# Optimization experiments

Hardware: AMD Instinct MI355X
Metric: run time of the kernel (lower is better)

## Reference

```python
import jax, jax.numpy as jnp
import numpy as np

NUM_HEADS = 16
HEAD_DIM = 64  # hidden_size 1024 / 16 heads


def setup_inputs() -> dict:
    key = jax.random.key(0)
    ks = jax.random.split(key, 4)
    B, S, H = 2, 2048, 1024
    scale = 1.0 / np.sqrt(H)
    return {
        "hidden_states": jax.random.normal(ks[0], (B, S, H), dtype=jnp.float32),
        "attention_mask": jnp.zeros((B, 1, 1, S), dtype=jnp.float32),
        "Wq": jax.random.normal(ks[1], (H, H), dtype=jnp.float32) * scale,
        "bq": jnp.zeros((H,), dtype=jnp.float32),
        "Wk": jax.random.normal(ks[2], (H, H), dtype=jnp.float32) * scale,
        "bk": jnp.zeros((H,), dtype=jnp.float32),
        "Wv": jax.random.normal(ks[3], (H, H), dtype=jnp.float32) * scale,
        "bv": jnp.zeros((H,), dtype=jnp.float32),
    }


def reference(hidden_states, attention_mask, Wq, bq, Wk, bk, Wv, bv):
    B, S, H = hidden_states.shape
    h, d = NUM_HEADS, HEAD_DIM

    def heads(x):  # [B,S,H] -> [B,h,S,d]
        return x.reshape(B, S, h, d).transpose(0, 2, 1, 3)

    q = heads(hidden_states @ Wq + bq)
    k = heads(hidden_states @ Wk + bk)
    v = heads(hidden_states @ Wv + bv)

    # [B,h,S,S] scores, scaled then additive-masked (HF BERT semantics)
    scores = jnp.einsum("bhqd,bhkd->bhqk", q, k) / jnp.sqrt(jnp.float32(d))
    scores = scores + attention_mask
    probs = jax.nn.softmax(scores, axis=-1)  # dropout p=0 -> identity

    ctx = jnp.einsum("bhqk,bhkd->bhqd", probs, v)
    ctx = ctx.transpose(0, 2, 1, 3).reshape(B, S, H)
    return ctx
```

## Files before the change

kernel.cpp:

```cpp
#include <hip/hip_runtime.h>
#include <hip/hip_bf16.h>


#define SEQ   2048
#define HID   1024
#define NHEAD 16
#define HD    64
#define SD    ((size_t)SEQ * HD)

typedef __bf16 bf16x8 __attribute__((ext_vector_type(8)));
typedef float  f32x4  __attribute__((ext_vector_type(4)));

#define L2E 1.4426950408889634f
#define SOFT_OFF 16.0f

__device__ __forceinline__ unsigned short f2b(float f) {
    unsigned int x = __float_as_uint(f);
    x += 0x7FFFu + ((x >> 16) & 1u);
    return (unsigned short)(x >> 16);
}

__device__ __forceinline__ void gload16(const unsigned short* g,
                                        unsigned short* l) {
    __builtin_amdgcn_global_load_lds(
        (const __attribute__((address_space(1))) unsigned int*)g,
        (__attribute__((address_space(3))) unsigned int*)l, 16, 0, 0);
}

__global__ __launch_bounds__(256) void cvt_x_k(const float* __restrict__ X,
                                               unsigned short* __restrict__ Xb)
{
    const size_t i = ((size_t)blockIdx.x * 256 + threadIdx.x) * 4;
    const float4 v = *(const float4*)(X + i);
    ushort4 o;
    o.x = f2b(v.x); o.y = f2b(v.y); o.z = f2b(v.z); o.w = f2b(v.w);
    *(ushort4*)(Xb + i) = o;
}

__global__ __launch_bounds__(256) void cvt_w_k(
    const float* __restrict__ Wq, const float* __restrict__ Wk,
    const float* __restrict__ Wv, unsigned short* __restrict__ Wtb)
{
    __shared__ __align__(16) unsigned short T[64][68];
    const int z = blockIdx.z;
    const float* __restrict__ W = (z == 0) ? Wq : (z == 1) ? Wk : Wv;
    const int k0 = blockIdx.x * 64, n0 = blockIdx.y * 64;
    const int tid = threadIdx.x;
    #pragma unroll
    for (int it = 0; it < 16; ++it) {
        const int idx = 256 * it + tid;
        const int r = idx >> 6, c = idx & 63;
        T[c][r] = f2b(W[(size_t)(k0 + r) * HID + n0 + c]);
    }
    __syncthreads();
    unsigned short* dst = Wtb + (size_t)z * HID * HID;
    #pragma unroll
    for (int it = 0; it < 4; ++it) {
        const int idx = 256 * it + tid;
        const int n = idx >> 4, c4 = (idx & 15) * 4;
        *(ushort4*)(dst + (size_t)(n0 + n) * HID + k0 + c4) = *(ushort4*)&T[n][c4];
    }
}

__global__ __launch_bounds__(256) void qkv_gemm_fused(
    const unsigned short* __restrict__ Xb, const unsigned short* __restrict__ Wtb,
    const float* __restrict__ bq, const float* __restrict__ bk,
    const float* __restrict__ bv, unsigned short* __restrict__ scratch)
{
    __shared__ __align__(16) unsigned char pool[40960];
    unsigned short (*Xs)[128][32] = (unsigned short (*)[128][32])pool;
    unsigned short (*Ws)[3][64][32] = (unsigned short (*)[3][64][32])(pool + 16384);

    const int orig = blockIdx.x;
    const int wg = ((orig & 7) << 6) + (orig >> 3);
    const int m0 = (wg & 31) * 128, n0 = (wg >> 5) * 64;

    const int tid = threadIdx.x, w = tid >> 6, lane = tid & 63;
    const int ln = lane & 15, quad = lane >> 4;
    const int wr = (w >> 1) * 64;
    const int wc = (w & 1) * 32;

    f32x4 acc[3][4][2];
    #pragma unroll
    for (int z = 0; z < 3; ++z)
        #pragma unroll
        for (int i = 0; i < 4; ++i)
            #pragma unroll
            for (int j = 0; j < 2; ++j) acc[z][i][j] = (f32x4){0.f, 0.f, 0.f, 0.f};

    #define STAGE(BUF, K0) { \
        _Pragma("unroll") for (int j = 0; j < 2; ++j) { \
            const int L = w * 128 + j * 64 + lane; \
            unsigned short* l = &Xs[BUF][0][0] + (size_t)(w * 128 + j * 64) * 8; \
            gload16(Xb + (size_t)(m0 + (L >> 2)) * HID + (K0) + (L & 3) * 8, l); \
        } \
        _Pragma("unroll") for (int j = 0; j < 3; ++j) { \
            const int L = w * 192 + j * 64 + lane; \
            const int z_ = L >> 8, r_ = (L & 255) >> 2, c_ = (L & 3) * 8; \
            unsigned short* l = &Ws[BUF][0][0][0] + (size_t)(w * 192 + j * 64) * 8; \
            gload16(Wtb + (size_t)z_ * HID * HID + (size_t)(n0 + r_) * HID + (K0) + c_, l); \
        } }

    STAGE(0, 0);

    int cur = 0;
    for (int k0 = 0; k0 < HID; k0 += 32) {
        __syncthreads();
        if (k0 + 32 < HID) {
            const int nxt = cur ^ 1;
            STAGE(nxt, k0 + 32);
        }

        bf16x8 am[4];
        #pragma unroll
        for (int t = 0; t < 4; ++t)
            am[t] = *(const bf16x8*)&Xs[cur][wr + t * 16 + ln][quad * 8];
        #pragma unroll
        for (int z = 0; z < 3; ++z) {
            bf16x8 bn[2];
            #pragma unroll
            for (int n = 0; n < 2; ++n)
                bn[n] = *(const bf16x8*)&Ws[cur][z][wc + n * 16 + ln][quad * 8];
            #pragma unroll
            for (int mt = 0; mt < 4; ++mt)
                #pragma unroll
                for (int nt = 0; nt < 2; ++nt)
                    acc[z][mt][nt] = __builtin_amdgcn_mfma_f32_16x16x32_bf16(
                        am[mt], bn[nt], acc[z][mt][nt], 0, 0, 0);
        }
        cur ^= 1;
    }
    #undef STAGE

    __syncthreads();
    const int b = m0 >> 11;
    const int srow0 = (m0 + wr) & (SEQ - 1);
    const int head = (n0 + wc) >> 6;
    const int dimb = (n0 + wc) & 63;

    unsigned short (*EtQ)[36] = (unsigned short (*)[36])(pool + (size_t)w * 4352);
    #pragma unroll
    for (int z = 0; z < 2; ++z) {
        const float* __restrict__ Bp = (z == 0) ? bq : bk;
        float bias[2];
        #pragma unroll
        for (int nt = 0; nt < 2; ++nt) bias[nt] = Bp[n0 + wc + nt * 16 + ln];
        #pragma unroll
        for (int half = 0; half < 2; ++half) {
            #pragma unroll
            for (int mt2 = 0; mt2 < 2; ++mt2) {
                const int mt = half * 2 + mt2;
                #pragma unroll
                for (int nt = 0; nt < 2; ++nt)
                    #pragma unroll
                    for (int r = 0; r < 4; ++r)
                        EtQ[mt2 * 16 + quad * 4 + r][nt * 16 + ln] =
                            f2b(acc[z][mt][nt][r] + bias[nt]);
            }
            #pragma unroll
            for (int it = 0; it < 4; ++it) {
                const int row = it * 8 + (lane >> 3), c4 = (lane & 7) * 4;
                *(ushort4*)(scratch +
                    ((size_t)(z * 32 + b * NHEAD + head) * SEQ + srow0
                     + half * 32 + row) * HD + dimb + c4) =
                    *(const ushort4*)&EtQ[row][c4];
            }
        }
    }
    {
        unsigned short (*EtV)[68] = (unsigned short (*)[68])(pool + (size_t)w * 4352);
        float bias[2];
        #pragma unroll
        for (int nt = 0; nt < 2; ++nt) bias[nt] = bv[n0 + wc + nt * 16 + ln];
        #pragma unroll
        for (int nt = 0; nt < 2; ++nt)
            #pragma unroll
            for (int mt = 0; mt < 4; ++mt) {
                ushort4 o;
                o.x = f2b(acc[2][mt][nt][0] + bias[nt]);
                o.y = f2b(acc[2][mt][nt][1] + bias[nt]);
                o.z = f2b(acc[2][mt][nt][2] + bias[nt]);
                o.w = f2b(acc[2][mt][nt][3] + bias[nt]);
                *(ushort4*)&EtV[nt * 16 + ln][mt * 16 + quad * 4] = o;
            }
        #pragma unroll
        for (int it = 0; it < 8; ++it) {
            const int d = it * 4 + quad, s4 = ln * 4;
            *(ushort4*)(scratch +
                ((size_t)(64 + b * NHEAD + head) * HD + dimb + d) * SEQ
                + srow0 + s4) = *(const ushort4*)&EtV[d][s4];
        }
    }
}

__device__ __forceinline__ void gemm_epilogue(
    f32x4 acc[4][4], const float* __restrict__ Bp,
    unsigned short* __restrict__ scratch, unsigned short (*Et)[68],
    int z, int m0, int n0, int wr, int wc, int ln, int quad)
{
    const int b = m0 >> 11;
    const int srow0 = (m0 + wr) & (SEQ - 1);
    const int head = (n0 + wc) >> 6;
    __syncthreads();

    if (z == 2) {
        #pragma unroll
        for (int half = 0; half < 2; ++half) {
            #pragma unroll
            for (int nt2 = 0; nt2 < 2; ++nt2) {
                const int nt = half * 2 + nt2;
                const float bias = Bp[n0 + wc + nt * 16 + ln];
                #pragma unroll
                for (int mt = 0; mt < 4; ++mt) {
                    ushort4 o;
                    o.x = f2b(acc[mt][nt][0] + bias);
                    o.y = f2b(acc[mt][nt][1] + bias);
                    o.z = f2b(acc[mt][nt][2] + bias);
                    o.w = f2b(acc[mt][nt][3] + bias);
                    *(ushort4*)&Et[nt2 * 16 + ln][mt * 16 + quad * 4] = o;
                }
            }
            __syncthreads();
            #pragma unroll
            for (int it = 0; it < 8; ++it) {
                const int d = it * 4 + quad, s4 = ln * 4;
                *(ushort4*)(scratch +
                    ((size_t)(64 + b * NHEAD + head) * HD + half * 32 + d) * SEQ
                    + srow0 + s4) = *(const ushort4*)&Et[d][s4];
            }
            __syncthreads();
        }
    } else {
        #pragma unroll
        for (int half = 0; half < 2; ++half) {
            #pragma unroll
            for (int mt2 = 0; mt2 < 2; ++mt2) {
                const int mt = half * 2 + mt2;
                #pragma unroll
                for (int nt = 0; nt < 4; ++nt) {
                    const float bias = Bp[n0 + wc + nt * 16 + ln];
                    #pragma unroll
                    for (int r = 0; r < 4; ++r)
                        Et[mt2 * 16 + quad * 4 + r][nt * 16 + ln] =
                            f2b(acc[mt][nt][r] + bias);
                }
            }
            __syncthreads();
            #pragma unroll
            for (int it = 0; it < 8; ++it) {
                const int r = it * 4 + quad, c4 = ln * 4;
                *(ushort4*)(scratch +
                    ((size_t)(z * 32 + b * NHEAD + head) * SEQ + srow0
                     + half * 32 + r) * HD + c4) = *(const ushort4*)&Et[r][c4];
            }
            __syncthreads();
        }
    }
}

__global__ __launch_bounds__(256) void qkv_gemm_fp32(
    const float* __restrict__ X,
    const float* __restrict__ Wq, const float* __restrict__ bq,
    const float* __restrict__ Wk, const float* __restrict__ bk,
    const float* __restrict__ Wv, const float* __restrict__ bv,
    unsigned short* __restrict__ scratch)
{
    __shared__ __align__(16) unsigned char pool[20480];
    unsigned short (*Xs)[40] = (unsigned short (*)[40])pool;
    unsigned short (*Wt)[40] = (unsigned short (*)[40])(pool + 10240);

    const int z = blockIdx.z;
    const float* __restrict__ W  = (z == 0) ? Wq : (z == 1) ? Wk : Wv;
    const float* __restrict__ Bp = (z == 0) ? bq : (z == 1) ? bk : bv;

    const int tid = threadIdx.x, w = tid >> 6, lane = tid & 63;
    const int ln = lane & 15, quad = lane >> 4;
    const int wr = (w >> 1) * 64, wc = (w & 1) * 64;
    const int m0 = blockIdx.x * 128, n0 = blockIdx.y * 128;

    const int xr = tid >> 3, xc = (tid & 7) * 4;
    const int wkr = tid >> 5, wnc = (tid & 31) * 4;

    f32x4 acc[4][4];
    #pragma unroll
    for (int i = 0; i < 4; ++i)
        #pragma unroll
        for (int j = 0; j < 4; ++j) acc[i][j] = (f32x4){0.f, 0.f, 0.f, 0.f};

    for (int k0 = 0; k0 < HID; k0 += 32) {
        __syncthreads();
        #pragma unroll
        for (int it = 0; it < 4; ++it) {
            const int r = xr + 32 * it;
            const float4 xv = *(const float4*)(X + (size_t)(m0 + r) * HID + k0 + xc);
            ushort4 xb;
            xb.x = f2b(xv.x); xb.y = f2b(xv.y); xb.z = f2b(xv.z); xb.w = f2b(xv.w);
            *(ushort4*)&Xs[r][xc] = xb;
            const int kr = wkr + 8 * it;
            const float4 wv = *(const float4*)(W + (size_t)(k0 + kr) * HID + n0 + wnc);
            Wt[wnc + 0][kr] = f2b(wv.x);
            Wt[wnc + 1][kr] = f2b(wv.y);
            Wt[wnc + 2][kr] = f2b(wv.z);
            Wt[wnc + 3][kr] = f2b(wv.w);
        }
        __syncthreads();
        bf16x8 am[4], bn[4];
        #pragma unroll
        for (int t = 0; t < 4; ++t) {
            am[t] = *(const bf16x8*)&Xs[wr + t * 16 + ln][quad * 8];
            bn[t] = *(const bf16x8*)&Wt[wc + t * 16 + ln][quad * 8];
        }
        #pragma unroll
        for (int mt = 0; mt < 4; ++mt)
            #pragma unroll
            for (int nt = 0; nt < 4; ++nt)
                acc[mt][nt] = __builtin_amdgcn_mfma_f32_16x16x32_bf16(
                    am[mt], bn[nt], acc[mt][nt], 0, 0, 0);
    }
    unsigned short (*Et)[68] = (unsigned short (*)[68])(pool + (size_t)w * 4352);
    gemm_epilogue(acc, Bp, scratch, Et, z, m0, n0, wr, wc, ln, quad);
}

__global__ __launch_bounds__(256) void attn_mfma(
    const unsigned short* __restrict__ scratch,
    const float* __restrict__ mask,
    float* __restrict__ out)
{
    __shared__ __align__(16) unsigned char smem[37888];
    unsigned short (*Ks)[64][72] = (unsigned short (*)[64][72])smem;
    unsigned short (*Vt)[64][72] = (unsigned short (*)[64][72])(smem + 18432);
    float* lrbuf = (float*)(smem + 36864);
    float (*OA)[68] = (float (*)[68])smem;
    float (*OB)[68] = (float (*)[68])(smem + 18432);

    const int orig = blockIdx.x;
    const int wg = ((orig & 7) << 7) + (orig >> 3);
    const int qt = wg & 31;
    const int bh = wg >> 5;
    const int b = bh >> 4, head = bh & 15;

    const unsigned short* __restrict__ Qp  = scratch + (size_t)bh * SD;
    const unsigned short* __restrict__ Kp  = scratch + (size_t)(32 + bh) * SD;
    const unsigned short* __restrict__ Vtp = scratch + (size_t)(64 + bh) * SD;
    const float* __restrict__ maskp = mask + b * SEQ;

    const int tid = threadIdx.x, w = tid >> 6, lane = tid & 63;
    const int ln = lane & 15, quad = lane >> 4;
    const int wk0 = w * 16;

    bf16x8 qb[4][2];
    #pragma unroll
    for (int t = 0; t < 4; ++t)
        #pragma unroll
        for (int h = 0; h < 2; ++h)
            qb[t][h] = *(const bf16x8*)(Qp +
                (size_t)(qt * 64 + t * 16 + ln) * HD + h * 32 + quad * 8);

    f32x4 O[4][4];
    #pragma unroll
    for (int i = 0; i < 4; ++i)
        #pragma unroll
        for (int j = 0; j < 4; ++j) O[i][j] = (f32x4){0.f, 0.f, 0.f, 0.f};
    float lr[4] = {0.f, 0.f, 0.f, 0.f};

    const int sr8 = tid >> 3, sc8 = (tid & 7) * 8;

    {
        uint4 a = *(const uint4*)(Kp + (size_t)sr8 * HD + sc8);
        uint4 c = *(const uint4*)(Kp + (size_t)(sr8 + 32) * HD + sc8);
        uint4 d = *(const uint4*)(Vtp + (size_t)sr8 * SEQ + sc8);
        uint4 e = *(const uint4*)(Vtp + (size_t)(sr8 + 32) * SEQ + sc8);
        *(uint4*)&Ks[0][sr8][sc8]      = a;
        *(uint4*)&Ks[0][sr8 + 32][sc8] = c;
        *(uint4*)&Vt[0][sr8][sc8]      = d;
        *(uint4*)&Vt[0][sr8 + 32][sc8] = e;
    }
    uint4 kg0 = *(const uint4*)(Kp + (size_t)(64 + sr8) * HD + sc8);
    uint4 kg1 = *(const uint4*)(Kp + (size_t)(64 + sr8 + 32) * HD + sc8);
    uint4 vg0 = *(const uint4*)(Vtp + (size_t)sr8 * SEQ + 64 + sc8);
    uint4 vg1 = *(const uint4*)(Vtp + (size_t)(sr8 + 32) * SEQ + 64 + sc8);
    __syncthreads();

    const float cc = 0.125f * L2E;

    for (int kt = 0; kt < 32; ++kt) {
        const int cur = kt & 1;
        if (kt < 31) {
            *(uint4*)&Ks[cur ^ 1][sr8][sc8]      = kg0;
            *(uint4*)&Ks[cur ^ 1][sr8 + 32][sc8] = kg1;
            *(uint4*)&Vt[cur ^ 1][sr8][sc8]      = vg0;
            *(uint4*)&Vt[cur ^ 1][sr8 + 32][sc8] = vg1;
        }
        if (kt < 30) {
            const int kn = kt + 2;
            kg0 = *(const uint4*)(Kp + (size_t)(kn * 64 + sr8) * HD + sc8);
            kg1 = *(const uint4*)(Kp + (size_t)(kn * 64 + sr8 + 32) * HD + sc8);
            vg0 = *(const uint4*)(Vtp + (size_t)sr8 * SEQ + kn * 64 + sc8);
            vg1 = *(const uint4*)(Vtp + (size_t)(sr8 + 32) * SEQ + kn * 64 + sc8);
        }

        const bf16x8 ka0 = *(const bf16x8*)&Ks[cur][wk0 + ln][quad * 8];
        const bf16x8 ka1 = *(const bf16x8*)&Ks[cur][wk0 + ln][32 + quad * 8];

        uint2 vl[4];
        #pragma unroll
        for (int dg = 0; dg < 4; ++dg)
            vl[dg] = *(const uint2*)&Vt[cur][dg * 16 + ln][wk0 + quad * 4];

        f32x4 s[4];
        #pragma unroll
        for (int t = 0; t < 4; ++t) {
            f32x4 a = (f32x4){0.f, 0.f, 0.f, 0.f};
            a = __builtin_amdgcn_mfma_f32_16x16x32_bf16(ka0, qb[t][0], a, 0, 0, 0);
            a = __builtin_amdgcn_mfma_f32_16x16x32_bf16(ka1, qb[t][1], a, 0, 0, 0);
            s[t] = a;
        }

        const float4 mk4 = *(const float4*)(maskp + kt * 64 + wk0 + quad * 4);
        const float b0 = fmaf(mk4.x, L2E, -SOFT_OFF);
        const float b1 = fmaf(mk4.y, L2E, -SOFT_OFF);
        const float b2 = fmaf(mk4.z, L2E, -SOFT_OFF);
        const float b3 = fmaf(mk4.w, L2E, -SOFT_OFF);

        bf16x8 pb[4];
        #pragma unroll
        for (int t = 0; t < 4; ++t) {
            const float p0 = exp2f(fmaf(s[t][0], cc, b0));
            const float p1 = exp2f(fmaf(s[t][1], cc, b1));
            const float p2 = exp2f(fmaf(s[t][2], cc, b2));
            const float p3 = exp2f(fmaf(s[t][3], cc, b3));
            lr[t] += (p0 + p1) + (p2 + p3);
            unsigned int w0, w1;
            asm("v_cvt_pk_bf16_f32 %0, %1, %2" : "=v"(w0) : "v"(p0), "v"(p1));
            asm("v_cvt_pk_bf16_f32 %0, %1, %2" : "=v"(w1) : "v"(p2), "v"(p3));
            uint4 pu; pu.x = w0; pu.y = w1; pu.z = w0; pu.w = w1;
            pb[t] = *(bf16x8*)&pu;
        }

        #pragma unroll
        for (int dg = 0; dg < 4; ++dg) {
            uint4 vu; vu.x = vl[dg].x; vu.y = vl[dg].y; vu.z = 0u; vu.w = 0u;
            const bf16x8 va = *(bf16x8*)&vu;
            #pragma unroll
            for (int t = 0; t < 4; ++t)
                O[dg][t] = __builtin_amdgcn_mfma_f32_16x16x32_bf16(
                    va, pb[t], O[dg][t], 0, 0, 0);
        }

        __syncthreads();
    }

    #pragma unroll
    for (int t = 0; t < 4; ++t) {
        lr[t] += __shfl_xor(lr[t], 16);
        lr[t] += __shfl_xor(lr[t], 32);
    }
    if (quad == 0) {
        #pragma unroll
        for (int t = 0; t < 4; ++t) lrbuf[w * 64 + t * 16 + ln] = lr[t];
    }

    #define O_WRITE(BUF) { \
        _Pragma("unroll") for (int dg = 0; dg < 4; ++dg) \
        _Pragma("unroll") for (int t = 0; t < 4; ++t) \
            *(float4*)&BUF[t * 16 + ln][dg * 16 + quad * 4] = \
                *(float4*)&O[dg][t]; }
    #define O_ADD(BUF) { \
        _Pragma("unroll") for (int dg = 0; dg < 4; ++dg) \
        _Pragma("unroll") for (int t = 0; t < 4; ++t) { \
            const float4 x = *(const float4*)&BUF[t * 16 + ln][dg * 16 + quad * 4]; \
            O[dg][t][0] += x.x; O[dg][t][1] += x.y; \
            O[dg][t][2] += x.z; O[dg][t][3] += x.w; } }

    if (w == 1) O_WRITE(OA);
    if (w == 3) O_WRITE(OB);
    __syncthreads();
    if (w == 0) O_ADD(OA);
    if (w == 2) O_ADD(OB);
    __syncthreads();
    if (w == 2) O_WRITE(OA);
    __syncthreads();
    if (w == 0) { O_ADD(OA); O_WRITE(OA); }
    __syncthreads();

    #pragma unroll
    for (int it = 0; it < 4; ++it) {
        const int r = (tid >> 4) + 16 * it, c4 = (tid & 15) * 4;
        const float lrt = lrbuf[r] + lrbuf[64 + r] + lrbuf[128 + r] + lrbuf[192 + r];
        const float inv = 1.0f / lrt;
        float4 v = *(const float4*)&OA[r][c4];
        v.x *= inv; v.y *= inv; v.z *= inv; v.w *= inv;
        *(float4*)(out + ((size_t)b * SEQ + qt * 64 + r) * HID + head * HD + c4) = v;
    }
    #undef O_WRITE
    #undef O_ADD
}

extern "C" void kernel_launch(void* const* d_in, const int* in_sizes, int n_in,
                              void* d_out, int out_size, void* d_ws, size_t ws_size,
                              hipStream_t stream) {
    const float* X    = (const float*)d_in[0];
    const float* mask = (const float*)d_in[1];
    const float* Wq   = (const float*)d_in[2];
    const float* bq   = (const float*)d_in[3];
    const float* Wk   = (const float*)d_in[4];
    const float* bk   = (const float*)d_in[5];
    const float* Wv   = (const float*)d_in[6];
    const float* bv   = (const float*)d_in[7];

    unsigned short* scratch = (unsigned short*)d_ws;
    float* out = (float*)d_out;

    const bool big = (ws_size >= (40ull << 20));
    if (big) {
        unsigned short* Xb  = scratch + 96 * SD;
        unsigned short* Wtb = Xb + (size_t)2 * SEQ * HID;
        cvt_x_k<<<4096, 256, 0, stream>>>(X, Xb);
        cvt_w_k<<<dim3(16, 16, 3), 256, 0, stream>>>(Wq, Wk, Wv, Wtb);
        qkv_gemm_fused<<<512, 256, 0, stream>>>(
            Xb, Wtb, bq, bk, bv, scratch);
    } else {
        qkv_gemm_fp32<<<dim3(32, 8, 3), 256, 0, stream>>>(
            X, Wq, bq, Wk, bk, Wv, bv, scratch);
    }
    attn_mfma<<<1024, 256, 0, stream>>>(scratch, mask, out);
}
```

Baseline: 195.1 us.

## Fuse input/weight conversion kernels and deepen QKV GEMM LDS pipeline to four buffers

Merges the two fp32-to-bf16 conversion kernels into a single launch that splits work by block index, removing one kernel launch and its gap. The QKV GEMM moves from a double-buffered K=32 loop to a four-buffer ring that loads two 32-wide stages ahead and computes two per barrier, halving the number of barriers. LDS use doubles to 80KB, which may reduce how many blocks fit per CU.

```diff
diff --git a/kernel.cpp b/kernel.cpp
--- a/kernel.cpp
+++ b/kernel.cpp
@@ -27,25 +27,27 @@
         (__attribute__((address_space(3))) unsigned int*)l, 16, 0, 0);
 }
 
-__global__ __launch_bounds__(256) void cvt_x_k(const float* __restrict__ X,
-                                               unsigned short* __restrict__ Xb)
-{
-    const size_t i = ((size_t)blockIdx.x * 256 + threadIdx.x) * 4;
-    const float4 v = *(const float4*)(X + i);
-    ushort4 o;
-    o.x = f2b(v.x); o.y = f2b(v.y); o.z = f2b(v.z); o.w = f2b(v.w);
-    *(ushort4*)(Xb + i) = o;
-}
-
-__global__ __launch_bounds__(256) void cvt_w_k(
+__global__ __launch_bounds__(256) void cvt_fused(
+    const float* __restrict__ X, unsigned short* __restrict__ Xb,
     const float* __restrict__ Wq, const float* __restrict__ Wk,
     const float* __restrict__ Wv, unsigned short* __restrict__ Wtb)
 {
     __shared__ __align__(16) unsigned short T[64][68];
-    const int z = blockIdx.z;
+    const int bid = blockIdx.x;
+    const int tid = threadIdx.x;
+    if (bid < 4096) {
+        const size_t i = ((size_t)bid * 256 + tid) * 4;
+        const float4 v = *(const float4*)(X + i);
+        ushort4 o;
+        o.x = f2b(v.x); o.y = f2b(v.y); o.z = f2b(v.z); o.w = f2b(v.w);
+        *(ushort4*)(Xb + i) = o;
+        return;
+    }
+    const int wb = bid - 4096;
+    const int z = wb >> 8;
+    const int rem = wb & 255;
+    const int k0 = (rem >> 4) * 64, n0 = (rem & 15) * 64;
     const float* __restrict__ W = (z == 0) ? Wq : (z == 1) ? Wk : Wv;
-    const int k0 = blockIdx.x * 64, n0 = blockIdx.y * 64;
-    const int tid = threadIdx.x;
     #pragma unroll
     for (int it = 0; it < 16; ++it) {
         const int idx = 256 * it + tid;
@@ -67,9 +69,9 @@
     const float* __restrict__ bq, const float* __restrict__ bk,
     const float* __restrict__ bv, unsigned short* __restrict__ scratch)
 {
-    __shared__ __align__(16) unsigned char pool[40960];
-    unsigned short (*Xs)[128][32] = (unsigned short (*)[128][32])pool;
-    unsigned short (*Ws)[3][64][32] = (unsigned short (*)[3][64][32])(pool + 16384);
+    __shared__ __align__(16) unsigned char pool[81920];
+    unsigned short (*Xs)[128][32]    = (unsigned short (*)[128][32])pool;
+    unsigned short (*Ws)[3][64][32]  = (unsigned short (*)[3][64][32])(pool + 32768);
 
     const int orig = blockIdx.x;
     const int wg = ((orig & 7) << 6) + (orig >> 3);
@@ -102,33 +104,37 @@
         } }
 
     STAGE(0, 0);
+    STAGE(1, 32);
 
     int cur = 0;
-    for (int k0 = 0; k0 < HID; k0 += 32) {
+    for (int k0 = 0; k0 < HID; k0 += 64) {
         __syncthreads();
-        if (k0 + 32 < HID) {
-            const int nxt = cur ^ 1;
-            STAGE(nxt, k0 + 32);
-        }
-
-        bf16x8 am[4];
-        #pragma unroll
-        for (int t = 0; t < 4; ++t)
-            am[t] = *(const bf16x8*)&Xs[cur][wr + t * 16 + ln][quad * 8];
-        #pragma unroll
-        for (int z = 0; z < 3; ++z) {
-            bf16x8 bn[2];
-            #pragma unroll
-            for (int n = 0; n < 2; ++n)
-                bn[n] = *(const bf16x8*)&Ws[cur][z][wc + n * 16 + ln][quad * 8];
-            #pragma unroll
-            for (int mt = 0; mt < 4; ++mt)
+        if (k0 + 64 < HID) {
+            STAGE(((cur + 2) & 3), k0 + 64);
+            STAGE(((cur + 3) & 3), k0 + 96);
+        }
+        #pragma unroll
+        for (int kk = 0; kk < 2; ++kk) {
+            const int bi = (cur + kk) & 3;
+            bf16x8 am[4];
+            #pragma unroll
+            for (int t = 0; t < 4; ++t)
+                am[t] = *(const bf16x8*)&Xs[bi][wr + t * 16 + ln][quad * 8];
+            #pragma unroll
+            for (int z = 0; z < 3; ++z) {
+                bf16x8 bn[2];
                 #pragma unroll
-                for (int nt = 0; nt < 2; ++nt)
-                    acc[z][mt][nt] = __builtin_amdgcn_mfma_f32_16x16x32_bf16(
-                        am[mt], bn[nt], acc[z][mt][nt], 0, 0, 0);
-        }
-        cur ^= 1;
+                for (int n = 0; n < 2; ++n)
+                    bn[n] = *(const bf16x8*)&Ws[bi][z][wc + n * 16 + ln][quad * 8];
+                #pragma unroll
+                for (int mt = 0; mt < 4; ++mt)
+                    #pragma unroll
+                    for (int nt = 0; nt < 2; ++nt)
+                        acc[z][mt][nt] = __builtin_amdgcn_mfma_f32_16x16x32_bf16(
+                            am[mt], bn[nt], acc[z][mt][nt], 0, 0, 0);
+            }
+        }
+        cur = (cur + 2) & 3;
     }
     #undef STAGE
 
@@ -515,8 +521,7 @@
     if (big) {
         unsigned short* Xb  = scratch + 96 * SD;
         unsigned short* Wtb = Xb + (size_t)2 * SEQ * HID;
-        cvt_x_k<<<4096, 256, 0, stream>>>(X, Xb);
-        cvt_w_k<<<dim3(16, 16, 3), 256, 0, stream>>>(Wq, Wk, Wv, Wtb);
+        cvt_fused<<<4864, 256, 0, stream>>>(X, Xb, Wq, Wk, Wv, Wtb);
         qkv_gemm_fused<<<512, 256, 0, stream>>>(
             Xb, Wtb, bq, bk, bv, scratch);
     } else {
```

Result: no change. 196.9 us (+0.9%).
